# Optimization experiments

Hardware: AMD Instinct MI355X
Metric: run time of the kernel (lower is better)

Reference implementation:

```python
import jax, jax.numpy as jnp
import numpy as np

N = 4096          # number_of_node
DIN = 3           # dim_input (forced: fc1 expects N*dim_input == N*3 after last stage)
DOUT = 4          # dim_output
DACT = N          # dim_action defaults to number_of_node
B = 128


def setup_inputs() -> dict:
    key = jax.random.key(0)
    ks = jax.random.split(key, 12)
    X = jax.random.normal(ks[0], (B, N * DIN), dtype=jnp.float32)
    adj = jax.random.uniform(ks[1], (N, N), dtype=jnp.float32)
    def lin(kw, kb, fan_in, fan_out):
        bound = 1.0 / np.sqrt(fan_in)
        W = jax.random.uniform(kw, (fan_in, fan_out), minval=-bound, maxval=bound, dtype=jnp.float32)
        b = jax.random.uniform(kb, (fan_out,), minval=-bound, maxval=bound, dtype=jnp.float32)
        return W, b
    W1, b1 = lin(ks[2], ks[3], DIN, 4)
    W2, b2 = lin(ks[4], ks[5], 4, DOUT)
    W3, b3 = lin(ks[6], ks[7], DOUT, 3)
    Wfc, bfc = lin(ks[8], ks[9], N * DIN, 54)
    Wout, bout = lin(ks[10], ks[11], 54, DACT)
    return {"X": X, "adj": adj, "W1": W1, "b1": b1, "W2": W2, "b2": b2,
            "W3": W3, "b3": b3, "Wfc": Wfc, "bfc": bfc, "Wout": Wout, "bout": bout}


def reference(X, adj, W1, b1, W2, b2, W3, b3, Wfc, bfc, Wout, bout):
    # X: [B, N*DIN] -> [B, N, DIN]
    h = X.reshape(X.shape[0], N, DIN)
    # three (adj @ h) aggregations fused with tiny Linear + ReLU
    h = jax.nn.relu(jnp.einsum('nm,bmf->bnf', adj, h) @ W1 + b1)   # [B,N,4]
    h = jax.nn.relu(jnp.einsum('nm,bmf->bnf', adj, h) @ W2 + b2)   # [B,N,DOUT]
    h = jax.nn.relu(jnp.einsum('nm,bmf->bnf', adj, h) @ W3 + b3)   # [B,N,3]
    flat = h.reshape(h.shape[0], -1)                               # [B, N*3]
    hid = jax.nn.relu(flat @ Wfc + bfc)                            # [B, 54]
    q_value = hid @ Wout + bout                                    # [B, DACT]
    return q_value
```

## Files before the change

kernel.cpp:

```cpp
#include <hip/hip_runtime.h>


typedef __bf16 bf16x8 __attribute__((ext_vector_type(8)));
typedef float  f32x4  __attribute__((ext_vector_type(4)));

#define N_NODE 4096
#define BATCH  128

__device__ __forceinline__ void async_copy16(const void* gsrc, void* ldst) {
    __builtin_amdgcn_global_load_lds(
        (const __attribute__((address_space(1))) void*)gsrc,
        (__attribute__((address_space(3))) void*)ldst,
        16, 0, 0);
}

__global__ __launch_bounds__(256) void prep_k(const float* __restrict__ adj,
                                              __bf16* __restrict__ adjB,
                                              const float* __restrict__ X,
                                              const float* __restrict__ W1,
                                              __bf16* __restrict__ G0,
                                              float* __restrict__ hid_acc) {
    const int blk = blockIdx.x, tx = threadIdx.x;
    if (blk < 8192) {
        const size_t i = (size_t)blk * 256 + tx;
        const float4* a4 = (const float4*)adj;
        float4 u = a4[i * 2];
        float4 v = a4[i * 2 + 1];
        bf16x8 o = { (__bf16)u.x, (__bf16)u.y, (__bf16)u.z, (__bf16)u.w,
                     (__bf16)v.x, (__bf16)v.y, (__bf16)v.z, (__bf16)v.w };
        *(bf16x8*)(adjB + i * 8) = o;
    } else if (blk < 9216) {
        const int g = (blk - 8192) * 256 + tx;
        const int lp = g & 63, cbg = (g >> 6) & 31, kc = g >> 11;
        const int c = cbg * 16 + (lp & 15);
        const int b = c >> 2, f = c & 3;
        const float w0 = W1[0 * 4 + f], w1 = W1[1 * 4 + f], w2 = W1[2 * 4 + f];
        const int mb = kc * 32 + ((lp >> 4) & 3) * 8;
        const float* Xb = X + (size_t)b * 12288 + (size_t)mb * 3;
        bf16x8 o;
#pragma unroll
        for (int j = 0; j < 8; ++j) {
            const float v = Xb[j * 3 + 0] * w0 + Xb[j * 3 + 1] * w1 + Xb[j * 3 + 2] * w2;
            o[j] = (__bf16)v;
        }
        *(bf16x8*)(G0 + (size_t)g * 8) = o;
    } else {
        const int i = (blk - 9216) * 256 + tx;
        if (i < BATCH * 54) hid_acc[i] = 0.f;
    }
}

template <int MODE>
__global__ __launch_bounds__(512, 2) void gcn_k(const __bf16* __restrict__ A,
                                                const __bf16* __restrict__ Bp,
                                                const float* __restrict__ Wa,
                                                const float* __restrict__ ba,
                                                const float* __restrict__ Wb,
                                                __bf16* __restrict__ Op,
                                                float* __restrict__ H3out) {
    __shared__ __align__(16) unsigned char smem[65536];
    const int tx = threadIdx.x;
    const int wave = tx >> 6, lane = tx & 63;
    const int quad = lane >> 4, lr = lane & 15;
    const int wm = wave >> 2, wk = wave & 3;

    const int l = blockIdx.x;
    const int xcd = l & 7, s = l >> 3;
    const int mi = xcd * 4 + (s & 3), ci = s >> 2;
    const int m0 = mi * 128, c0 = ci * 64;

    const __bf16* gA[4];
#pragma unroll
    for (int q = 0; q < 4; ++q) {
        const int c = q * 512 + tx;
        const int r = c >> 4, p = c & 15;
        const int lk = (p - r) & 15;
        gA[q] = A + (size_t)(m0 + r) * 4096 + lk * 8;
    }
    const __bf16* gB[4];
#pragma unroll
    for (int j = 0; j < 4; ++j)
        gB[j] = Bp + ((size_t)((wk * 32 + (ci * 4 + j)) * 64 + lane)) * 8;

    const int posw = ((wk * 4 + quad + lr) & 15) * 8;
    int foffA[4];
#pragma unroll
    for (int i = 0; i < 4; ++i) foffA[i] = (wm * 64 + i * 16 + lr) * 128 + posw;

    f32x4 acc[4][4] = {};
    bf16x8 bv0[4], bv1[4];

#pragma unroll
    for (int q = 0; q < 4; ++q)
        async_copy16(gA[q], smem + q * 8192 + tx * 16);
#pragma unroll
    for (int j = 0; j < 4; ++j) bv0[j] = *(const bf16x8*)(gB[j]);

#define GCN_ITER(KT, CUR, NXT)                                                 \
    {                                                                          \
        asm volatile("s_waitcnt vmcnt(0)" ::: "memory");                       \
        __builtin_amdgcn_s_barrier();                                          \
        const __bf16* Ab = (const __bf16*)(smem + ((KT) & 1) * 32768);         \
        bf16x8 af[4];                                                          \
        _Pragma("unroll") for (int i = 0; i < 4; ++i)                          \
            af[i] = *(const bf16x8*)(Ab + foffA[i]);                           \
        if ((KT) + 1 < 32) {                                                   \
            const int bo = (((KT) + 1) & 1) * 32768;                           \
            const int k0 = ((KT) + 1) * 128;                                   \
            _Pragma("unroll") for (int q = 0; q < 4; ++q)                      \
                async_copy16(gA[q] + k0, smem + bo + q * 8192 + tx * 16);      \
            _Pragma("unroll") for (int j = 0; j < 4; ++j)                      \
                NXT[j] = *(const bf16x8*)(gB[j] + ((KT) + 1) * 65536);         \
        }                                                                      \
        __builtin_amdgcn_s_setprio(1);                                         \
        _Pragma("unroll") for (int i = 0; i < 4; ++i)                          \
            _Pragma("unroll") for (int j = 0; j < 4; ++j)                      \
                acc[i][j] = __builtin_amdgcn_mfma_f32_16x16x32_bf16(           \
                    af[i], CUR[j], acc[i][j], 0, 0, 0);                        \
        __builtin_amdgcn_s_setprio(0);                                         \
    }

    for (int kt = 0; kt < 32; kt += 2) {
        GCN_ITER(kt, bv0, bv1)
        GCN_ITER(kt + 1, bv1, bv0)
    }
#undef GCN_ITER

    __syncthreads();
    float* part = (float*)smem;
    if (wk & 1) {
        float* slot = part + (wm * 2 + (wk >> 1)) * 4096;
#pragma unroll
        for (int t = 0; t < 16; ++t)
            *(f32x4*)(slot + lane * 64 + ((t + lane) & 15) * 4) = acc[t >> 2][t & 3];
    }
    __syncthreads();
    if (!(wk & 1)) {
        const float* slot = part + (wm * 2 + (wk >> 1)) * 4096;
#pragma unroll
        for (int t = 0; t < 16; ++t)
            acc[t >> 2][t & 3] += *(const f32x4*)(slot + lane * 64 + ((t + lane) & 15) * 4);
    }
    __syncthreads();
    if (wk == 2) {
        float* slot = part + wm * 4096;
#pragma unroll
        for (int t = 0; t < 16; ++t)
            *(f32x4*)(slot + lane * 64 + ((t + lane) & 15) * 4) = acc[t >> 2][t & 3];
    }
    __syncthreads();
    if (wk == 0) {
#pragma unroll
        for (int t = 0; t < 16; ++t)
            acc[t >> 2][t & 3] += *(const f32x4*)(part + wm * 4096 + lane * 64 + ((t + lane) & 15) * 4);
    }
    __syncthreads();
    float* Ct = part;
    if (wk == 0) {
#pragma unroll
        for (int i = 0; i < 4; ++i)
#pragma unroll
            for (int j = 0; j < 4; ++j)
#pragma unroll
                for (int r = 0; r < 4; ++r)
                    Ct[(wm * 64 + i * 16 + quad * 4 + r) * 65 + j * 16 + lr] = acc[i][j][r];
    }
    __syncthreads();

    if (MODE == 0) {
#pragma unroll
        for (int it = 0; it < 2; ++it) {
            const int g = it * 512 + tx;
            const int lp = g & 63, cbl = (g >> 6) & 3, kcl = g >> 8;
            const int cl = cbl * 16 + (lp & 15);
            const float bf = ba[cl & 3];
            const int mb = kcl * 32 + ((lp >> 4) & 3) * 8;
            bf16x8 o;
#pragma unroll
            for (int j = 0; j < 8; ++j)
                o[j] = (__bf16)fmaxf(Ct[(mb + j) * 65 + cl] + bf, 0.f);
            *(bf16x8*)(Op + ((size_t)((mi * 4 + kcl) * 32 + (ci * 4 + cbl)) * 64 + lp) * 8) = o;
        }
    } else if (MODE == 1) {
        float W2l[16], W3l[12], bl2[4];
#pragma unroll
        for (int i = 0; i < 16; ++i) W2l[i] = Wa[i];
#pragma unroll
        for (int i = 0; i < 12; ++i) W3l[i] = Wb[i];
#pragma unroll
        for (int i = 0; i < 4; ++i) bl2[i] = ba[i];
#pragma unroll
        for (int it = 0; it < 2; ++it) {
            const int g = it * 512 + tx;
            const int lp = g & 63, cbl = (g >> 6) & 3, kcl = g >> 8;
            const int cl = cbl * 16 + (lp & 15);
            const int bloc = cl >> 2, f3 = cl & 3;
            const int mb = kcl * 32 + ((lp >> 4) & 3) * 8;
            bf16x8 o;
#pragma unroll
            for (int j = 0; j < 8; ++j) {
                const float* row = &Ct[(mb + j) * 65 + bloc * 4];
                float v = 0.f;
                if (f3 < 3) {
#pragma unroll
                    for (int fo = 0; fo < 4; ++fo) {
                        const float tmp = fmaxf(row[0] * W2l[fo] + row[1] * W2l[4 + fo] +
                                                row[2] * W2l[8 + fo] + row[3] * W2l[12 + fo] +
                                                bl2[fo], 0.f);
                        const float w3a = W3l[fo * 3 + 0], w3b = W3l[fo * 3 + 1],
                                    w3c = W3l[fo * 3 + 2];
                        v += tmp * (f3 == 0 ? w3a : (f3 == 1 ? w3b : w3c));
                    }
                }
                o[j] = (__bf16)v;
            }
            *(bf16x8*)(Op + ((size_t)((mi * 4 + kcl) * 32 + (ci * 4 + cbl)) * 64 + lp) * 8) = o;
        }
    } else {
        const int m_l = tx & 127, cq = tx >> 7;
#pragma unroll
        for (int t = 0; t < 16; ++t) {
            const int cl = cq * 16 + t;
            const int c = c0 + cl, b = c >> 2, f = c & 3;
            if (f < 3)
                H3out[(size_t)(b * 3 + f) * N_NODE + m0 + m_l] =
                    fmaxf(Ct[m_l * 65 + cl] + ba[f], 0.f);
        }
    }
}

__global__ __launch_bounds__(256) void fc1p_k(const float* __restrict__ H3,
                                              const float* __restrict__ Wfc,
                                              float* __restrict__ hid_acc) {
    __shared__ float hs[16 * 192];
    __shared__ float red[4][16][64];
    const int tx = threadIdx.x;
    const int wv = tx >> 6, lane = tx & 63;
    const int n0 = blockIdx.x * 64;
    const int b0 = blockIdx.y * 16;

    for (int idx = tx; idx < 3072; idx += 256) {
        const int n = idx & 63, f = (idx >> 6) % 3, b = idx / 192;
        hs[idx] = H3[((size_t)((b0 + b) * 3 + f)) * N_NODE + n0 + n];
    }
    __syncthreads();

    float acc[16];
#pragma unroll
    for (int b = 0; b < 16; ++b) acc[b] = 0.f;
    if (lane < 54) {
        const int nb = wv * 16;
        for (int n = 0; n < 16; ++n) {
#pragma unroll
            for (int f = 0; f < 3; ++f) {
                const float w = Wfc[((size_t)(n0 + nb + n) * 3 + f) * 54 + lane];
#pragma unroll
                for (int b = 0; b < 16; ++b)
                    acc[b] += hs[b * 192 + f * 64 + nb + n] * w;
            }
        }
    }
#pragma unroll
    for (int b = 0; b < 16; ++b) red[wv][b][lane] = acc[b];
    __syncthreads();
    if (wv == 0 && lane < 54) {
        for (int b = 0; b < 16; ++b) {
            const float s = red[0][b][lane] + red[1][b][lane] +
                            red[2][b][lane] + red[3][b][lane];
            atomicAdd(&hid_acc[(b0 + b) * 54 + lane], s);
        }
    }
}

__global__ __launch_bounds__(256) void fc2_k(const float* __restrict__ hid_acc,
                                             const float* __restrict__ bfc,
                                             const float* __restrict__ Wout,
                                             const float* __restrict__ bout,
                                             float* __restrict__ out) {
    const int tx = threadIdx.x;
    const int a  = blockIdx.x * 256 + tx;
    const int b0 = blockIdx.y * 4;
    __shared__ float hs[4 * 54];
    if (tx < 216) {
        const int j = tx % 54;
        hs[tx] = fmaxf(hid_acc[b0 * 54 + tx] + bfc[j], 0.f);
    }
    __syncthreads();
    float a0 = 0.f, a1 = 0.f, a2 = 0.f, a3 = 0.f;
    for (int j = 0; j < 54; ++j) {
        float w = Wout[(size_t)j * N_NODE + a];
        a0 += hs[0 * 54 + j] * w;
        a1 += hs[1 * 54 + j] * w;
        a2 += hs[2 * 54 + j] * w;
        a3 += hs[3 * 54 + j] * w;
    }
    float bo = bout[a];
    out[(size_t)(b0 + 0) * N_NODE + a] = a0 + bo;
    out[(size_t)(b0 + 1) * N_NODE + a] = a1 + bo;
    out[(size_t)(b0 + 2) * N_NODE + a] = a2 + bo;
    out[(size_t)(b0 + 3) * N_NODE + a] = a3 + bo;
}

extern "C" void kernel_launch(void* const* d_in, const int* in_sizes, int n_in,
                              void* d_out, int out_size, void* d_ws, size_t ws_size,
                              hipStream_t stream) {
    const float* X    = (const float*)d_in[0];
    const float* adj  = (const float*)d_in[1];
    const float* W1   = (const float*)d_in[2];
    const float* b1   = (const float*)d_in[3];
    const float* W2   = (const float*)d_in[4];
    const float* b2   = (const float*)d_in[5];
    const float* W3   = (const float*)d_in[6];
    const float* b3   = (const float*)d_in[7];
    const float* Wfc  = (const float*)d_in[8];
    const float* bfc  = (const float*)d_in[9];
    const float* Wout = (const float*)d_in[10];
    const float* bout = (const float*)d_in[11];
    float* out = (float*)d_out;

    char* w = (char*)d_ws;
    __bf16* adjB = (__bf16*)w;
    __bf16* G0   = (__bf16*)(w + 33554432);
    __bf16* H1   = (__bf16*)(w + 33554432 + 4194304);
    __bf16* H2g  = (__bf16*)(w + 33554432 + 2 * 4194304);
    float*  H3   = (float*)(w + 33554432 + 3 * 4194304);
    float*  hid  = (float*)(w + 33554432 + 3 * 4194304 + 6291456);

    prep_k<<<9243, 256, 0, stream>>>(adj, adjB, X, W1, G0, hid);

    gcn_k<0><<<256, 512, 0, stream>>>(adjB, G0, nullptr, b1, nullptr, H1, nullptr);
    gcn_k<1><<<256, 512, 0, stream>>>(adjB, H1, W2, b2, W3, H2g, nullptr);
    gcn_k<2><<<256, 512, 0, stream>>>(adjB, H2g, nullptr, b3, nullptr, nullptr, H3);

    fc1p_k<<<dim3(64, 8), 256, 0, stream>>>(H3, Wfc, hid);
    fc2_k<<<dim3(16, 32), 256, 0, stream>>>(hid, bfc, Wout, bout, out);
}
```

Before: 248.3 us.

## Deepen GCN main-loop pipeline to four LDS stages with partial vmcnt waits

The K-loop moves from double-buffered to quad-buffered LDS, doubling shared memory to 128 KB and prefetching three tiles ahead. Waits become partial vmcnt waits instead of full drains, so global loads stay in flight across iterations and memory latency is better hidden. The reduction scratch layout also changes to a linear, conflict-free stride, and the output tile moves to a separate LDS region. In exchange, 128 KB of LDS per block likely allows only one 512-thread block per CU despite launch_bounds(512,2), which cuts occupancy, and the vmcnt counts must match the exact number of outstanding loads.

```diff
diff --git a/kernel.cpp b/kernel.cpp
--- a/kernel.cpp
+++ b/kernel.cpp
@@ -58,7 +58,7 @@
                                                 const float* __restrict__ Wb,
                                                 __bf16* __restrict__ Op,
                                                 float* __restrict__ H3out) {
-    __shared__ __align__(16) unsigned char smem[65536];
+    __shared__ __align__(16) unsigned char smem[131072];
     const int tx = threadIdx.x;
     const int wave = tx >> 6, lane = tx & 63;
     const int quad = lane >> 4, lr = lane & 15;
@@ -88,29 +88,39 @@
     for (int i = 0; i < 4; ++i) foffA[i] = (wm * 64 + i * 16 + lr) * 128 + posw;
 
     f32x4 acc[4][4] = {};
-    bf16x8 bv0[4], bv1[4];
-
-#pragma unroll
-    for (int q = 0; q < 4; ++q)
-        async_copy16(gA[q], smem + q * 8192 + tx * 16);
+    bf16x8 bv0[4], bv1[4], bv2[4], bv3[4];
+
+#pragma unroll
+    for (int q = 0; q < 4; ++q) async_copy16(gA[q], smem + q * 8192 + tx * 16);
 #pragma unroll
     for (int j = 0; j < 4; ++j) bv0[j] = *(const bf16x8*)(gB[j]);
-
-#define GCN_ITER(KT, CUR, NXT)                                                 \
+    asm volatile("" ::: "memory");
+#pragma unroll
+    for (int q = 0; q < 4; ++q) async_copy16(gA[q] + 128, smem + 32768 + q * 8192 + tx * 16);
+#pragma unroll
+    for (int j = 0; j < 4; ++j) bv1[j] = *(const bf16x8*)(gB[j] + 65536);
+    asm volatile("" ::: "memory");
+#pragma unroll
+    for (int q = 0; q < 4; ++q) async_copy16(gA[q] + 256, smem + 65536 + q * 8192 + tx * 16);
+#pragma unroll
+    for (int j = 0; j < 4; ++j) bv2[j] = *(const bf16x8*)(gB[j] + 131072);
+    asm volatile("" ::: "memory");
+
+#define GCN_STEP(KT, P, WAIT, PF, CUR, NXT)                                    \
     {                                                                          \
-        asm volatile("s_waitcnt vmcnt(0)" ::: "memory");                       \
+        asm volatile(WAIT ::: "memory");                                       \
         __builtin_amdgcn_s_barrier();                                          \
-        const __bf16* Ab = (const __bf16*)(smem + ((KT) & 1) * 32768);         \
+        const __bf16* Ab = (const __bf16*)(smem + (P) * 32768);                \
         bf16x8 af[4];                                                          \
         _Pragma("unroll") for (int i = 0; i < 4; ++i)                          \
             af[i] = *(const bf16x8*)(Ab + foffA[i]);                           \
-        if ((KT) + 1 < 32) {                                                   \
-            const int bo = (((KT) + 1) & 1) * 32768;                           \
-            const int k0 = ((KT) + 1) * 128;                                   \
+        if (PF) {                                                              \
+            const int nt_ = (KT) + 3;                                          \
+            unsigned char* bo_ = smem + (((P) + 3) & 3) * 32768;               \
             _Pragma("unroll") for (int q = 0; q < 4; ++q)                      \
-                async_copy16(gA[q] + k0, smem + bo + q * 8192 + tx * 16);      \
+                async_copy16(gA[q] + nt_ * 128, bo_ + q * 8192 + tx * 16);     \
             _Pragma("unroll") for (int j = 0; j < 4; ++j)                      \
-                NXT[j] = *(const bf16x8*)(gB[j] + ((KT) + 1) * 65536);         \
+                NXT[j] = *(const bf16x8*)(gB[j] + (size_t)nt_ * 65536);        \
         }                                                                      \
         __builtin_amdgcn_s_setprio(1);                                         \
         _Pragma("unroll") for (int i = 0; i < 4; ++i)                          \
@@ -120,42 +130,46 @@
         __builtin_amdgcn_s_setprio(0);                                         \
     }
 
-    for (int kt = 0; kt < 32; kt += 2) {
-        GCN_ITER(kt, bv0, bv1)
-        GCN_ITER(kt + 1, bv1, bv0)
-    }
-#undef GCN_ITER
+    for (int kt = 0; kt < 28; kt += 4) {
+        GCN_STEP(kt + 0, 0, "s_waitcnt vmcnt(16) lgkmcnt(0)", 1, bv0, bv3)
+        GCN_STEP(kt + 1, 1, "s_waitcnt vmcnt(16) lgkmcnt(0)", 1, bv1, bv0)
+        GCN_STEP(kt + 2, 2, "s_waitcnt vmcnt(16) lgkmcnt(0)", 1, bv2, bv1)
+        GCN_STEP(kt + 3, 3, "s_waitcnt vmcnt(16) lgkmcnt(0)", 1, bv3, bv2)
+    }
+    GCN_STEP(28, 0, "s_waitcnt vmcnt(16) lgkmcnt(0)", 1, bv0, bv3)
+    GCN_STEP(29, 1, "s_waitcnt vmcnt(16) lgkmcnt(0)", 0, bv1, bv0)
+    GCN_STEP(30, 2, "s_waitcnt vmcnt(8) lgkmcnt(0)",  0, bv2, bv1)
+    GCN_STEP(31, 3, "s_waitcnt vmcnt(0) lgkmcnt(0)",  0, bv3, bv2)
+#undef GCN_STEP
 
     __syncthreads();
     float* part = (float*)smem;
+    const int sb = (wm * 2 + (wk >> 1)) * 4096;
     if (wk & 1) {
-        float* slot = part + (wm * 2 + (wk >> 1)) * 4096;
 #pragma unroll
         for (int t = 0; t < 16; ++t)
-            *(f32x4*)(slot + lane * 64 + ((t + lane) & 15) * 4) = acc[t >> 2][t & 3];
+            *(f32x4*)(part + sb + t * 256 + lane * 4) = acc[t >> 2][t & 3];
     }
     __syncthreads();
     if (!(wk & 1)) {
-        const float* slot = part + (wm * 2 + (wk >> 1)) * 4096;
 #pragma unroll
         for (int t = 0; t < 16; ++t)
-            acc[t >> 2][t & 3] += *(const f32x4*)(slot + lane * 64 + ((t + lane) & 15) * 4);
+            acc[t >> 2][t & 3] += *(const f32x4*)(part + sb + t * 256 + lane * 4);
     }
     __syncthreads();
     if (wk == 2) {
-        float* slot = part + wm * 4096;
 #pragma unroll
         for (int t = 0; t < 16; ++t)
-            *(f32x4*)(slot + lane * 64 + ((t + lane) & 15) * 4) = acc[t >> 2][t & 3];
+            *(f32x4*)(part + wm * 4096 + t * 256 + lane * 4) = acc[t >> 2][t & 3];
     }
     __syncthreads();
     if (wk == 0) {
 #pragma unroll
         for (int t = 0; t < 16; ++t)
-            acc[t >> 2][t & 3] += *(const f32x4*)(part + wm * 4096 + lane * 64 + ((t + lane) & 15) * 4);
-    }
-    __syncthreads();
-    float* Ct = part;
+            acc[t >> 2][t & 3] += *(const f32x4*)(part + wm * 4096 + t * 256 + lane * 4);
+    }
+    __syncthreads();
+    float* Ct = (float*)(smem + 65536);
     if (wk == 0) {
 #pragma unroll
         for (int i = 0; i < 4; ++i)
```

Result: faster. 232.0 us (-6.6%).
